# Performance work log

Measured on AMD Instinct MI355X. Metric: run time of the kernel, lower is better.

The kernel has to match this reference:

```python
import jax, jax.numpy as jnp
import numpy as np

QUERY_DIM = 1024
HIDDEN_DIM = 1024


def setup_inputs() -> dict:
    key = jax.random.key(0)
    k1, k2, k3, k4 = jax.random.split(key, 4)
    query = jax.random.normal(k1, (8, 2048, QUERY_DIM), dtype=jnp.float32)
    info = jax.random.normal(k2, (8, 2048, HIDDEN_DIM), dtype=jnp.float32)
    # nn.Linear params: weight [out, in], bias [out]
    bound = 1.0 / np.sqrt(QUERY_DIM)
    W = jax.random.uniform(k3, (HIDDEN_DIM, QUERY_DIM), jnp.float32, -bound, bound)
    b = jax.random.uniform(k4, (HIDDEN_DIM,), jnp.float32, -bound, bound)
    return {"query": query, "info": info, "W": W, "b": b}


def reference(query, info, W, b):
    # Eval mode: dropout is identity.
    # projected query: [B, S, hidden]
    q = jnp.einsum("bsq,hq->bsh", query, W) + b
    # unscaled attention scores over info rows: [B, S, M]
    scores = jax.nn.softmax(jnp.einsum("bsh,bmh->bsm", q, info), axis=-1)
    # weighted sum of info: [B, S, hidden]
    return jnp.einsum("bsm,bmh->bsh", scores, info)
```

## Files before the change

### kernel.cpp

```cpp
#include <hip/hip_runtime.h>

#define DEVI __device__ __forceinline__

typedef __attribute__((ext_vector_type(4))) float f32x4;
typedef __attribute__((ext_vector_type(8))) short bf16x8;

typedef const unsigned __attribute__((address_space(1))) as1_u32;
typedef unsigned __attribute__((address_space(3))) as3_u32;

DEVI unsigned fbits(float x){ union{float f;unsigned u;} v; v.f=x; return v.u; }
DEVI float bitsf(unsigned u){ union{unsigned u;float f;} v; v.u=u; return v.f; }
DEVI short bf_rne(float x){ unsigned u=fbits(x); u += 0x7fffu + ((u>>16)&1u); return (short)(u>>16); }

DEVI unsigned pack_hi2(unsigned u0, unsigned u1){
#if __has_builtin(__builtin_amdgcn_perm)
  return __builtin_amdgcn_perm(u1, u0, 0x07060302u);
#else
  return (u0 >> 16) | (u1 & 0xffff0000u);
#endif
}
DEVI unsigned pack_rne2(float a, float b){
  return (unsigned)(unsigned short)bf_rne(a) | ((unsigned)(unsigned short)bf_rne(b) << 16);
}

DEVI void gload16(const short* g, short* s){
  __builtin_amdgcn_global_load_lds((as1_u32*)g, (as3_u32*)s, 16, 0, 0);
}

#define SBAR() { __builtin_amdgcn_sched_barrier(0); asm volatile("" ::: "memory"); \
                 __builtin_amdgcn_s_barrier(); __builtin_amdgcn_sched_barrier(0); }

#define MF(a,b,c) __builtin_amdgcn_mfma_f32_16x16x32_bf16(a,b,c,0,0,0)
#define MROW(M, x) \
  acc[M][0] = MF(x, bb0, acc[M][0]); \
  acc[M][1] = MF(x, bb1, acc[M][1]); \
  acc[M][2] = MF(x, bb2, acc[M][2]); \
  acc[M][3] = MF(x, bb3, acc[M][3]);

__global__ __launch_bounds__(256)
void k_split(const float* __restrict__ in, short* __restrict__ hi,
             short* __restrict__ lo, const long n4)
{
  long i = (long)blockIdx.x*256 + threadIdx.x;
  const long stride = (long)gridDim.x*256;
  for (; i < n4; i += stride){
    const float4 v = ((const float4*)in)[i];
    const unsigned u0=fbits(v.x), u1=fbits(v.y), u2=fbits(v.z), u3=fbits(v.w);
    ((uint2*)hi)[i] = make_uint2(pack_hi2(u0,u1), pack_hi2(u2,u3));
    const float l0 = v.x - bitsf(u0 & 0xffff0000u);
    const float l1 = v.y - bitsf(u1 & 0xffff0000u);
    const float l2 = v.z - bitsf(u2 & 0xffff0000u);
    const float l3 = v.w - bitsf(u3 & 0xffff0000u);
    ((uint2*)lo)[i] = make_uint2(pack_rne2(l0,l1), pack_rne2(l2,l3));
  }
}

template<int NPHASE, bool BIAS, bool SPLIT_OUT>
__global__ __launch_bounds__(512, 2)
void k_gemm(const short* __restrict__ Ah, const short* __restrict__ Al,
            const short* __restrict__ Bh, const short* __restrict__ Bl,
            void* __restrict__ Cv, const float* __restrict__ bias,
            const int K, const int lda, const int ldb, const int ldc,
            const long sAz, const long sBz, const long sCz, const int loOff)
{
  __shared__ short LDS[65536];

  const int tid = threadIdx.x;
  const int w = tid >> 6, l = tid & 63;
  const int wr = w >> 2, wc = w & 3;
  const int fr = l & 15, h4 = l >> 4;
  const long bz = blockIdx.z;

  const int nwg = gridDim.x * gridDim.y;
  const int xy  = blockIdx.y * gridDim.x + blockIdx.x;
  const int q8  = nwg >> 3;
  const int sw  = (xy & 7) * q8 + (xy >> 3);
  const int bx  = sw % gridDim.x;
  const int by  = sw / gridDim.x;

  const size_t aOff = (size_t)bz*sAz + (size_t)bx*256*lda;
  const size_t bOff = (size_t)bz*sBz + (size_t)by*256*ldb;

  const int sch = (((l & 7) ^ ((l >> 3) & 7)) << 3);
  const int rA0 = wr*128 + (w & 3)*8 + (l >> 3);
  int aoffg[4];
#pragma unroll
  for (int q2 = 0; q2 < 4; ++q2) aoffg[q2] = (rA0 + 32*q2)*lda;
  const int rB0 = wc*64 + (w >> 2)*8 + (l >> 3);
  int boffg[4];
#pragma unroll
  for (int j2 = 0; j2 < 4; ++j2) boffg[j2] = (rB0 + 16*j2)*ldb;
  const int dAu = wr*8192 + (w & 3)*512;
  const int dBu = 16384 + wc*4096 + (w >> 2)*512;

  const int rbA = (wr*128 + fr)*64;
  const int rbB = 16384 + (wc*64 + fr)*64;
  const int c08 = ((h4     ) ^ (l & 7)) << 3;
  const int c18 = ((h4 + 4 ) ^ (l & 7)) << 3;

  f32x4 acc[8][4];
#pragma unroll
  for (int m = 0; m < 8; ++m)
#pragma unroll
    for (int n = 0; n < 4; ++n){ acc[m][n][0]=0.f; acc[m][n][1]=0.f; acc[m][n][2]=0.f; acc[m][n][3]=0.f; }

  const short* Asrc = Ah + aOff + sch;
  const short* Bsrc = Bh + bOff + sch;
  int skt = 0, spass = 0;
  const int nkt = NPHASE * (K >> 6);

  {
    short* dB0 = LDS + dBu;
    short* dA0 = LDS + dAu;
    gload16(Bsrc + boffg[0], dB0);
    gload16(Bsrc + boffg[1], dB0 + 1024);
    gload16(Bsrc + boffg[2], dB0 + 2048);
    gload16(Bsrc + boffg[3], dB0 + 3072);
    gload16(Asrc + aoffg[0], dA0);
    gload16(Asrc + aoffg[1], dA0 + 2048);
    gload16(Asrc + aoffg[2], dA0 + 4096);
    gload16(Asrc + aoffg[3], dA0 + 6144);
  }
  skt = 64; Asrc += 64; Bsrc += 64;
  asm volatile("s_waitcnt vmcnt(2)" ::: "memory");
  SBAR();

#define ADVANCE()                                                            \
  { skt += 64;                                                               \
    if (skt == K){ skt = 0; ++spass;                                         \
      Asrc = ((NPHASE==3 && spass==1) ? Al : Ah) + aOff + sch;               \
      Bsrc = ((NPHASE==3 && spass==2) ? Bl : Bh) + bOff + sch;               \
    } else { Asrc += 64; Bsrc += 64; } }

#define TILE(CO, PF, VA, VB)                                                 \
{                                                                            \
  const short* pA = LDS + (CO) + rbA;                                        \
  const short* pB = LDS + (CO) + rbB;                                        \
  short* dAp = LDS + ((CO)^32768) + dAu;                                     \
  short* dBp = LDS + ((CO)^32768) + dBu;                                     \
  bf16x8 aA,aB,aC,aD, bb0,bb1,bb2,bb3;                                       \
                                            \
  if (PF){ gload16(Bsrc + boffg[0], dBp); gload16(Bsrc + boffg[1], dBp + 1024); } \
  bb0 = *(const bf16x8*)(pB +        c08);                                   \
  bb1 = *(const bf16x8*)(pB + 1024 + c08);                                   \
  bb2 = *(const bf16x8*)(pB + 2048 + c08);                                   \
  bb3 = *(const bf16x8*)(pB + 3072 + c08);                                   \
  aA  = *(const bf16x8*)(pA +        c08);                                   \
  aB  = *(const bf16x8*)(pA + 1024 + c08);                                   \
  aC  = *(const bf16x8*)(pA + 2048 + c08);                                   \
  aD  = *(const bf16x8*)(pA + 3072 + c08);                                   \
  SBAR();                                                                    \
  __builtin_amdgcn_s_setprio(1);                                             \
  MROW(0,aA) MROW(1,aB) MROW(2,aC) MROW(3,aD)                                \
  __builtin_amdgcn_s_setprio(0);                                             \
  asm volatile("s_waitcnt vmcnt(" VA ")" ::: "memory");                      \
  SBAR();                                                                    \
                                                    \
  if (PF){ gload16(Bsrc + boffg[2], dBp + 2048); gload16(Bsrc + boffg[3], dBp + 3072); } \
  aA = *(const bf16x8*)(pA + 4096 + c08);                                    \
  aB = *(const bf16x8*)(pA + 5120 + c08);                                    \
  aC = *(const bf16x8*)(pA + 6144 + c08);                                    \
  aD = *(const bf16x8*)(pA + 7168 + c08);                                    \
  SBAR();                                                                    \
  __builtin_amdgcn_s_setprio(1);                                             \
  MROW(4,aA) MROW(5,aB) MROW(6,aC) MROW(7,aD)                                \
  __builtin_amdgcn_s_setprio(0);                                             \
  SBAR();                                                                    \
                                            \
  if (PF){ gload16(Asrc + aoffg[0], dAp); gload16(Asrc + aoffg[1], dAp + 2048); } \
  bb0 = *(const bf16x8*)(pB +        c18);                                   \
  bb1 = *(const bf16x8*)(pB + 1024 + c18);                                   \
  bb2 = *(const bf16x8*)(pB + 2048 + c18);                                   \
  bb3 = *(const bf16x8*)(pB + 3072 + c18);                                   \
  aA  = *(const bf16x8*)(pA +        c18);                                   \
  aB  = *(const bf16x8*)(pA + 1024 + c18);                                   \
  aC  = *(const bf16x8*)(pA + 2048 + c18);                                   \
  aD  = *(const bf16x8*)(pA + 3072 + c18);                                   \
  SBAR();                                                                    \
  __builtin_amdgcn_s_setprio(1);                                             \
  MROW(0,aA) MROW(1,aB) MROW(2,aC) MROW(3,aD)                                \
  __builtin_amdgcn_s_setprio(0);                                             \
  SBAR();                                                                    \
                                                    \
  if (PF){ gload16(Asrc + aoffg[2], dAp + 4096); gload16(Asrc + aoffg[3], dAp + 6144); } \
  aA = *(const bf16x8*)(pA + 4096 + c18);                                    \
  aB = *(const bf16x8*)(pA + 5120 + c18);                                    \
  aC = *(const bf16x8*)(pA + 6144 + c18);                                    \
  aD = *(const bf16x8*)(pA + 7168 + c18);                                    \
  SBAR();                                                                    \
  __builtin_amdgcn_s_setprio(1);                                             \
  MROW(4,aA) MROW(5,aB) MROW(6,aC) MROW(7,aD)                                \
  __builtin_amdgcn_s_setprio(0);                                             \
  if (PF){ ADVANCE(); }                                                      \
  asm volatile("s_waitcnt vmcnt(" VB ")" ::: "memory");                      \
  SBAR();                                                                    \
}

#pragma unroll 1
  for (int it = 0; it < nkt - 2; it += 2){
    TILE(0,     1, "2", "2")
    TILE(32768, 1, "2", "2")
  }
  TILE(0,     1, "2", "2")
  TILE(32768, 0, "0", "0")

#undef TILE
#undef ADVANCE

  const int rr = h4*4;
  if constexpr (SPLIT_OUT){
    short* Ch = (short*)Cv + (size_t)bz*sCz
              + (size_t)(bx*256 + wr*128)*ldc + by*256 + wc*64;
    short* Cl = Ch + loOff;
#pragma unroll
    for (int n = 0; n < 4; ++n){
      const int col = n*16 + fr;
      const float bv = BIAS ? bias[by*256 + wc*64 + col] : 0.f;
#pragma unroll
      for (int m = 0; m < 8; ++m)
#pragma unroll
        for (int j = 0; j < 4; ++j){
          const float v = acc[m][n][j] + bv;
          const unsigned uh = fbits(v) & 0xffff0000u;
          const size_t idx = (size_t)(m*16 + rr + j)*ldc + col;
          Ch[idx] = (short)(uh >> 16);
          Cl[idx] = bf_rne(v - bitsf(uh));
        }
    }
  } else {
    float* C = (float*)Cv + (size_t)bz*sCz
             + (size_t)(bx*256 + wr*128)*ldc + by*256 + wc*64;
#pragma unroll
    for (int n = 0; n < 4; ++n){
      const int col = n*16 + fr;
      const float bv = BIAS ? bias[by*256 + wc*64 + col] : 0.f;
#pragma unroll
      for (int m = 0; m < 8; ++m)
#pragma unroll
        for (int j = 0; j < 4; ++j)
          C[(size_t)(m*16 + rr + j)*ldc + col] = acc[m][n][j] + bv;
    }
  }
}

__global__ __launch_bounds__(256)
void k_prep_info(const float* __restrict__ V, short* __restrict__ hi,
                 short* __restrict__ lo, short* __restrict__ T,
                 const int MM, const int DD, const long sVz, const long sTz)
{
  __shared__ float t[64][65];
  const float* Vb = V + (long)blockIdx.z*sVz;
  short* hb = hi + (long)blockIdx.z*sVz;
  short* lb = lo + (long)blockIdx.z*sVz;
  short* Tb = T  + (long)blockIdx.z*sTz;
  const int m0 = blockIdx.x*64, d0 = blockIdx.y*64;
  const int tid = threadIdx.x;
#pragma unroll
  for (int i = 0; i < 4; ++i){
    const int c = tid + 256*i;
    const int r = c >> 4, c4 = (c & 15)*4;
    const float4 v = *(const float4*)(Vb + (size_t)(m0 + r)*DD + d0 + c4);
    t[r][c4+0]=v.x; t[r][c4+1]=v.y; t[r][c4+2]=v.z; t[r][c4+3]=v.w;
    const unsigned u0=fbits(v.x), u1=fbits(v.y), u2=fbits(v.z), u3=fbits(v.w);
    const size_t gi = (size_t)(m0 + r)*DD + d0 + c4;
    *(uint2*)(hb + gi) = make_uint2(pack_hi2(u0,u1), pack_hi2(u2,u3));
    const float l0 = v.x - bitsf(u0 & 0xffff0000u);
    const float l1 = v.y - bitsf(u1 & 0xffff0000u);
    const float l2 = v.z - bitsf(u2 & 0xffff0000u);
    const float l3 = v.w - bitsf(u3 & 0xffff0000u);
    *(uint2*)(lb + gi) = make_uint2(pack_rne2(l0,l1), pack_rne2(l2,l3));
  }
  __syncthreads();
#pragma unroll
  for (int i = 0; i < 4; ++i){
    const int c = tid + 256*i;
    const int d = c >> 4, m4 = (c & 15)*4;
    short4 o;
    o.x = bf_rne(t[m4+0][d]); o.y = bf_rne(t[m4+1][d]);
    o.z = bf_rne(t[m4+2][d]); o.w = bf_rne(t[m4+3][d]);
    *(short4*)(Tb + (size_t)(d0 + d)*MM + m0 + m4) = o;
  }
}

__global__ __launch_bounds__(256)
void k_softmax_rows(float* __restrict__ Sb, const long sz)
{
  float* row = Sb + (long)blockIdx.y*sz + (long)blockIdx.x*2048;
  short* prow = (short*)row;
  const int tid = threadIdx.x;
  const int lane = tid & 63, wid = tid >> 6;

  const float4 v0 = *(const float4*)(row + tid*4);
  const float4 v1 = *(const float4*)(row + 1024 + tid*4);
  float x[8] = {v0.x, v0.y, v0.z, v0.w, v1.x, v1.y, v1.z, v1.w};

  float mx = x[0];
#pragma unroll
  for (int j = 1; j < 8; ++j) mx = fmaxf(mx, x[j]);
#pragma unroll
  for (int off = 32; off; off >>= 1) mx = fmaxf(mx, __shfl_xor(mx, off));

  __shared__ float red[8];
  if (lane == 0) red[wid] = mx;
  __syncthreads();
  mx = fmaxf(fmaxf(red[0], red[1]), fmaxf(red[2], red[3]));

  float e[8]; float s = 0.f;
#pragma unroll
  for (int j = 0; j < 8; ++j){ e[j] = __expf(x[j] - mx); s += e[j]; }
#pragma unroll
  for (int off = 32; off; off >>= 1) s += __shfl_xor(s, off);
  if (lane == 0) red[4 + wid] = s;
  __syncthreads();
  s = (red[4] + red[5]) + (red[6] + red[7]);
  const float inv = 1.0f / s;

  *(uint2*)(prow + tid*4)        = make_uint2(pack_rne2(e[0]*inv, e[1]*inv), pack_rne2(e[2]*inv, e[3]*inv));
  *(uint2*)(prow + 1024 + tid*4) = make_uint2(pack_rne2(e[4]*inv, e[5]*inv), pack_rne2(e[6]*inv, e[7]*inv));
}

extern "C" void kernel_launch(void* const* d_in, const int* in_sizes, int n_in,
                              void* d_out, int out_size, void* d_ws, size_t ws_size,
                              hipStream_t stream)
{
  const float* query = (const float*)d_in[0];
  const float* info  = (const float*)d_in[1];
  const float* Wm    = (const float*)d_in[2];
  const float* bias  = (const float*)d_in[3];
  float* out = (float*)d_out;

  const int B = 8, S = 2048, M = 2048, D = 1024;
  const size_t PB = (size_t)S * D;

  short* info_hi = (short*)d_ws;
  short* info_lo = info_hi + 16777216;
  short* infoT   = info_lo + 16777216;
  short* W_hi    = infoT   + 16777216;
  short* W_lo    = W_hi    + 1048576;
  float* Sbuf    = (float*)(W_lo + 1048576);
  const size_t sb = (size_t)S * M * sizeof(float);
  size_t avail = ws_size > 104857600ull ? ws_size - 104857600ull : 0;
  int nchunk = (int)(avail / sb); if (nchunk > 8) nchunk = 8; if (nchunk < 1) nchunk = 1;

  short* q_s = (short*)d_out;
  const long qBz = 2*(long)PB;
  const int  qLo = (int)PB;

  k_split<<<1024, 256, 0, stream>>>(Wm, W_hi, W_lo, (long)(D*D/4));

  int nb = 2*nchunk; if (nb > 8) nb = 8;
  for (int q0 = 0; q0 < B; q0 += nb){
    const int cur = (q0 + nb <= B) ? nb : (B - q0);
    short* qt_hi = (short*)Sbuf;
    short* qt_lo = qt_hi + (size_t)cur*PB;
    k_split<<<2048, 256, 0, stream>>>(query + (size_t)q0*PB, qt_hi, qt_lo,
                                      (long)((size_t)cur*PB/4));
    k_gemm<3, true, true><<<dim3(S/256, D/256, cur), 512, 0, stream>>>(
        qt_hi, qt_lo, W_hi, W_lo, q_s + (size_t)q0*qBz, bias,
        D, D, D, D, (long)PB, 0L, qBz, qLo);
  }

  k_prep_info<<<dim3(M/64, D/64, B), 256, 0, stream>>>(
      info, info_hi, info_lo, infoT, M, D, (long)PB, (long)PB);

  for (int b0 = 0; b0 < B; b0 += nchunk){
    const int cur = (b0 + nchunk <= B) ? nchunk : (B - b0);

    const short* qh = q_s + (size_t)b0*qBz;
    k_gemm<3, false, false><<<dim3(S/256, M/256, cur), 512, 0, stream>>>(
        qh, qh + qLo, info_hi + (size_t)b0*PB, info_lo + (size_t)b0*PB,
        Sbuf, nullptr, D, D, D, M, qBz, (long)PB, (long)S*M, 0);

    k_softmax_rows<<<dim3(S, cur), 256, 0, stream>>>(Sbuf, (long)S*M);

    k_gemm<1, false, false><<<dim3(S/256, D/256, cur), 512, 0, stream>>>(
        (const short*)Sbuf, nullptr, infoT + (size_t)b0*PB, nullptr,
        out + (size_t)b0*PB, nullptr, M, 2*M, M, D,
        (long)(2*(size_t)S*M), (long)PB, (long)PB, 0);
  }
}
```

Baseline: 450.6 us.

## Fuse three bf16 split passes into single K loop reusing LDS fragments

```diff
diff --git a/kernel.cpp b/kernel.cpp
--- a/kernel.cpp
+++ b/kernel.cpp
@@ -55,13 +55,13 @@
   }
 }
 
-template<int NPHASE, bool BIAS, bool SPLIT_OUT>
+template<bool BIAS, bool SPLIT_OUT>
 __global__ __launch_bounds__(512, 2)
-void k_gemm(const short* __restrict__ Ah, const short* __restrict__ Al,
-            const short* __restrict__ Bh, const short* __restrict__ Bl,
-            void* __restrict__ Cv, const float* __restrict__ bias,
-            const int K, const int lda, const int ldb, const int ldc,
-            const long sAz, const long sBz, const long sCz, const int loOff)
+void k_gemm3(const short* __restrict__ Ah, const short* __restrict__ Al,
+             const short* __restrict__ Bh, const short* __restrict__ Bl,
+             void* __restrict__ Cv, const float* __restrict__ bias,
+             const int K, const int lda, const int ldb, const int ldc,
+             const long sAz, const long sBz, const long sCz, const int loOff)
 {
   __shared__ short LDS[65536];
 
@@ -81,6 +81,172 @@
   const size_t aOff = (size_t)bz*sAz + (size_t)bx*256*lda;
   const size_t bOff = (size_t)bz*sBz + (size_t)by*256*ldb;
 
+  const int c0 = w*64 + l, c1 = c0 + 512;
+  const size_t a0 = (size_t)(c0 >> 2)*lda + (c0 & 3)*8;
+  const size_t a1 = (size_t)(c1 >> 2)*lda + (c1 & 3)*8;
+  const size_t b0 = (size_t)(c0 >> 2)*ldb + (c0 & 3)*8;
+  const size_t b1 = (size_t)(c1 >> 2)*ldb + (c1 & 3)*8;
+  const int dS0 = w*512, dS1 = 4096 + w*512;
+
+  const int rbA = (wr*128 + fr)*32 + h4*8;
+  const int rbB = 16384 + (wc*64 + fr)*32 + h4*8;
+
+  f32x4 acc[8][4];
+#pragma unroll
+  for (int m = 0; m < 8; ++m)
+#pragma unroll
+    for (int n = 0; n < 4; ++n){ acc[m][n][0]=0.f; acc[m][n][1]=0.f; acc[m][n][2]=0.f; acc[m][n][3]=0.f; }
+
+  const short* pAh = Ah + aOff;
+  const short* pAl = Al + aOff;
+  const short* pBh = Bh + bOff;
+  const short* pBl = Bl + bOff;
+
+  gload16(pAh + a0, LDS + dS0);
+  gload16(pAh + a1, LDS + dS1);
+  gload16(pBh + b0, LDS + 16384 + dS0);
+  gload16(pBh + b1, LDS + 16384 + dS1);
+  gload16(pAl + a0, LDS + 8192 + dS0);
+  gload16(pAl + a1, LDS + 8192 + dS1);
+  gload16(pBl + b0, LDS + 24576 + dS0);
+  gload16(pBl + b1, LDS + 24576 + dS1);
+  pAh += 32; pAl += 32; pBh += 32; pBl += 32;
+
+#define STEP3(CO, PF, V1, V2, V3)                                            \
+{                                                                            \
+  const short* pA = LDS + (CO) + rbA;                                        \
+  const short* pB = LDS + (CO) + rbB;                                        \
+  short* dst = LDS + ((CO) ^ 32768);                                         \
+  bf16x8 ah0,ah1,ah2,ah3,ah4,ah5,ah6,ah7, bb0,bb1,bb2,bb3;                   \
+                                                            \
+  asm volatile("s_waitcnt vmcnt(" V1 ")" ::: "memory");                      \
+  SBAR();                                                                    \
+  if (PF){ gload16(pAh + a0, dst + dS0);                                     \
+           gload16(pAh + a1, dst + dS1);                                     \
+           gload16(pBh + b0, dst + 16384 + dS0);                             \
+           gload16(pBh + b1, dst + 16384 + dS1); }                           \
+  bb0 = *(const bf16x8*)(pB);                                                \
+  bb1 = *(const bf16x8*)(pB + 512);                                          \
+  bb2 = *(const bf16x8*)(pB + 1024);                                         \
+  bb3 = *(const bf16x8*)(pB + 1536);                                         \
+  ah0 = *(const bf16x8*)(pA);                                                \
+  ah1 = *(const bf16x8*)(pA + 512);                                          \
+  ah2 = *(const bf16x8*)(pA + 1024);                                         \
+  ah3 = *(const bf16x8*)(pA + 1536);                                         \
+  ah4 = *(const bf16x8*)(pA + 2048);                                         \
+  ah5 = *(const bf16x8*)(pA + 2560);                                         \
+  ah6 = *(const bf16x8*)(pA + 3072);                                         \
+  ah7 = *(const bf16x8*)(pA + 3584);                                         \
+  __builtin_amdgcn_s_setprio(1);                                             \
+  MROW(0,ah0) MROW(1,ah1) MROW(2,ah2) MROW(3,ah3)                            \
+  MROW(4,ah4) MROW(5,ah5) MROW(6,ah6) MROW(7,ah7)                            \
+  __builtin_amdgcn_s_setprio(0);                                             \
+                                                            \
+  asm volatile("s_waitcnt vmcnt(" V2 ")" ::: "memory");                      \
+  SBAR();                                                                    \
+  if (PF){ gload16(pAl + a0, dst + 8192 + dS0);                              \
+           gload16(pAl + a1, dst + 8192 + dS1);                              \
+           gload16(pBl + b0, dst + 24576 + dS0);                             \
+           gload16(pBl + b1, dst + 24576 + dS1);                             \
+           pAh += 32; pAl += 32; pBh += 32; pBl += 32; }                     \
+  {                                                                          \
+    bf16x8 al0 = *(const bf16x8*)(pA + 8192);                                \
+    bf16x8 al1 = *(const bf16x8*)(pA + 8192 + 512);                          \
+    bf16x8 al2 = *(const bf16x8*)(pA + 8192 + 1024);                         \
+    bf16x8 al3 = *(const bf16x8*)(pA + 8192 + 1536);                         \
+    bf16x8 al4 = *(const bf16x8*)(pA + 8192 + 2048);                         \
+    bf16x8 al5 = *(const bf16x8*)(pA + 8192 + 2560);                         \
+    bf16x8 al6 = *(const bf16x8*)(pA + 8192 + 3072);                         \
+    bf16x8 al7 = *(const bf16x8*)(pA + 8192 + 3584);                         \
+    __builtin_amdgcn_s_setprio(1);                                           \
+    MROW(0,al0) MROW(1,al1) MROW(2,al2) MROW(3,al3)                          \
+    MROW(4,al4) MROW(5,al5) MROW(6,al6) MROW(7,al7)                          \
+    __builtin_amdgcn_s_setprio(0);                                           \
+  }                                                                          \
+                                                            \
+  asm volatile("s_waitcnt vmcnt(" V3 ")" ::: "memory");                      \
+  SBAR();                                                                    \
+  bb0 = *(const bf16x8*)(pB + 8192);                                         \
+  bb1 = *(const bf16x8*)(pB + 8192 + 512);                                   \
+  bb2 = *(const bf16x8*)(pB + 8192 + 1024);                                  \
+  bb3 = *(const bf16x8*)(pB + 8192 + 1536);                                  \
+  __builtin_amdgcn_s_setprio(1);                                             \
+  MROW(0,ah0) MROW(1,ah1) MROW(2,ah2) MROW(3,ah3)                            \
+  MROW(4,ah4) MROW(5,ah5) MROW(6,ah6) MROW(7,ah7)                            \
+  __builtin_amdgcn_s_setprio(0);                                             \
+}
+
+  const int nk = K >> 5;
+#pragma unroll 1
+  for (int it = 0; it < nk - 2; it += 2){
+    STEP3(0,     1, "4", "6", "8")
+    STEP3(32768, 1, "4", "6", "8")
+  }
+  STEP3(0,     1, "4", "6", "8")
+  STEP3(32768, 0, "4", "2", "0")
+
+#undef STEP3
+
+  const int rr = h4*4;
+  if constexpr (SPLIT_OUT){
+    short* Ch = (short*)Cv + (size_t)bz*sCz
+              + (size_t)(bx*256 + wr*128)*ldc + by*256 + wc*64;
+    short* Cl = Ch + loOff;
+#pragma unroll
+    for (int n = 0; n < 4; ++n){
+      const int col = n*16 + fr;
+      const float bv = BIAS ? bias[by*256 + wc*64 + col] : 0.f;
+#pragma unroll
+      for (int m = 0; m < 8; ++m)
+#pragma unroll
+        for (int j = 0; j < 4; ++j){
+          const float v = acc[m][n][j] + bv;
+          const unsigned uh = fbits(v) & 0xffff0000u;
+          const size_t idx = (size_t)(m*16 + rr + j)*ldc + col;
+          Ch[idx] = (short)(uh >> 16);
+          Cl[idx] = bf_rne(v - bitsf(uh));
+        }
+    }
+  } else {
+    float* C = (float*)Cv + (size_t)bz*sCz
+             + (size_t)(bx*256 + wr*128)*ldc + by*256 + wc*64;
+#pragma unroll
+    for (int n = 0; n < 4; ++n){
+      const int col = n*16 + fr;
+      const float bv = BIAS ? bias[by*256 + wc*64 + col] : 0.f;
+#pragma unroll
+      for (int m = 0; m < 8; ++m)
+#pragma unroll
+        for (int j = 0; j < 4; ++j)
+          C[(size_t)(m*16 + rr + j)*ldc + col] = acc[m][n][j] + bv;
+    }
+  }
+}
+
+__global__ __launch_bounds__(512, 2)
+void k_gemm1(const short* __restrict__ Ah, const short* __restrict__ Bh,
+             void* __restrict__ Cv,
+             const int K, const int lda, const int ldb, const int ldc,
+             const long sAz, const long sBz, const long sCz)
+{
+  __shared__ short LDS[65536];
+
+  const int tid = threadIdx.x;
+  const int w = tid >> 6, l = tid & 63;
+  const int wr = w >> 2, wc = w & 3;
+  const int fr = l & 15, h4 = l >> 4;
+  const long bz = blockIdx.z;
+
+  const int nwg = gridDim.x * gridDim.y;
+  const int xy  = blockIdx.y * gridDim.x + blockIdx.x;
+  const int q8  = nwg >> 3;
+  const int sw  = (xy & 7) * q8 + (xy >> 3);
+  const int bx  = sw % gridDim.x;
+  const int by  = sw / gridDim.x;
+
+  const size_t aOff = (size_t)bz*sAz + (size_t)bx*256*lda;
+  const size_t bOff = (size_t)bz*sBz + (size_t)by*256*ldb;
+
   const int sch = (((l & 7) ^ ((l >> 3) & 7)) << 3);
   const int rA0 = wr*128 + (w & 3)*8 + (l >> 3);
   int aoffg[4];
@@ -106,8 +272,6 @@
 
   const short* Asrc = Ah + aOff + sch;
   const short* Bsrc = Bh + bOff + sch;
-  int skt = 0, spass = 0;
-  const int nkt = NPHASE * (K >> 6);
 
   {
     short* dB0 = LDS + dBu;
@@ -121,16 +285,9 @@
     gload16(Asrc + aoffg[2], dA0 + 4096);
     gload16(Asrc + aoffg[3], dA0 + 6144);
   }
-  skt = 64; Asrc += 64; Bsrc += 64;
+  Asrc += 64; Bsrc += 64;
   asm volatile("s_waitcnt vmcnt(2)" ::: "memory");
   SBAR();
-
-#define ADVANCE()                                                            \
-  { skt += 64;                                                               \
-    if (skt == K){ skt = 0; ++spass;                                         \
-      Asrc = ((NPHASE==3 && spass==1) ? Al : Ah) + aOff + sch;               \
-      Bsrc = ((NPHASE==3 && spass==2) ? Bl : Bh) + bOff + sch;               \
-    } else { Asrc += 64; Bsrc += 64; } }
 
 #define TILE(CO, PF, VA, VB)                                                 \
 {                                                                            \
@@ -139,7 +296,6 @@
   short* dAp = LDS + ((CO)^32768) + dAu;                                     \
   short* dBp = LDS + ((CO)^32768) + dBu;                                     \
   bf16x8 aA,aB,aC,aD, bb0,bb1,bb2,bb3;                                       \
-                                            \
   if (PF){ gload16(Bsrc + boffg[0], dBp); gload16(Bsrc + boffg[1], dBp + 1024); } \
   bb0 = *(const bf16x8*)(pB +        c08);                                   \
   bb1 = *(const bf16x8*)(pB + 1024 + c08);                                   \
@@ -155,7 +311,6 @@
   __builtin_amdgcn_s_setprio(0);                                             \
   asm volatile("s_waitcnt vmcnt(" VA ")" ::: "memory");                      \
   SBAR();                                                                    \
-                                                    \
   if (PF){ gload16(Bsrc + boffg[2], dBp + 2048); gload16(Bsrc + boffg[3], dBp + 3072); } \
   aA = *(const bf16x8*)(pA + 4096 + c08);                                    \
   aB = *(const bf16x8*)(pA + 5120 + c08);                                    \
@@ -166,7 +321,6 @@
   MROW(4,aA) MROW(5,aB) MROW(6,aC) MROW(7,aD)                                \
   __builtin_amdgcn_s_setprio(0);                                             \
   SBAR();                                                                    \
-                                            \
   if (PF){ gload16(Asrc + aoffg[0], dAp); gload16(Asrc + aoffg[1], dAp + 2048); } \
   bb0 = *(const bf16x8*)(pB +        c18);                                   \
   bb1 = *(const bf16x8*)(pB + 1024 + c18);                                   \
@@ -181,7 +335,6 @@
   MROW(0,aA) MROW(1,aB) MROW(2,aC) MROW(3,aD)                                \
   __builtin_amdgcn_s_setprio(0);                                             \
   SBAR();                                                                    \
-                                                    \
   if (PF){ gload16(Asrc + aoffg[2], dAp + 4096); gload16(Asrc + aoffg[3], dAp + 6144); } \
   aA = *(const bf16x8*)(pA + 4096 + c18);                                    \
   aB = *(const bf16x8*)(pA + 5120 + c18);                                    \
@@ -191,11 +344,12 @@
   __builtin_amdgcn_s_setprio(1);                                             \
   MROW(4,aA) MROW(5,aB) MROW(6,aC) MROW(7,aD)                                \
   __builtin_amdgcn_s_setprio(0);                                             \
-  if (PF){ ADVANCE(); }                                                      \
+  if (PF){ Asrc += 64; Bsrc += 64; }                                         \
   asm volatile("s_waitcnt vmcnt(" VB ")" ::: "memory");                      \
   SBAR();                                                                    \
 }
 
+  const int nkt = K >> 6;
 #pragma unroll 1
   for (int it = 0; it < nkt - 2; it += 2){
     TILE(0,     1, "2", "2")
@@ -205,41 +359,18 @@
   TILE(32768, 0, "0", "0")
 
 #undef TILE
-#undef ADVANCE
 
   const int rr = h4*4;
-  if constexpr (SPLIT_OUT){
-    short* Ch = (short*)Cv + (size_t)bz*sCz
-              + (size_t)(bx*256 + wr*128)*ldc + by*256 + wc*64;
-    short* Cl = Ch + loOff;
-#pragma unroll
-    for (int n = 0; n < 4; ++n){
-      const int col = n*16 + fr;
-      const float bv = BIAS ? bias[by*256 + wc*64 + col] : 0.f;
-#pragma unroll
-      for (int m = 0; m < 8; ++m)
-#pragma unroll
-        for (int j = 0; j < 4; ++j){
-          const float v = acc[m][n][j] + bv;
-          const unsigned uh = fbits(v) & 0xffff0000u;
-          const size_t idx = (size_t)(m*16 + rr + j)*ldc + col;
-          Ch[idx] = (short)(uh >> 16);
-          Cl[idx] = bf_rne(v - bitsf(uh));
-        }
-    }
-  } else {
-    float* C = (float*)Cv + (size_t)bz*sCz
-             + (size_t)(bx*256 + wr*128)*ldc + by*256 + wc*64;
-#pragma unroll
-    for (int n = 0; n < 4; ++n){
-      const int col = n*16 + fr;
-      const float bv = BIAS ? bias[by*256 + wc*64 + col] : 0.f;
-#pragma unroll
-      for (int m = 0; m < 8; ++m)
-#pragma unroll
-        for (int j = 0; j < 4; ++j)
-          C[(size_t)(m*16 + rr + j)*ldc + col] = acc[m][n][j] + bv;
-    }
+  float* C = (float*)Cv + (size_t)bz*sCz
+           + (size_t)(bx*256 + wr*128)*ldc + by*256 + wc*64;
+#pragma unroll
+  for (int n = 0; n < 4; ++n){
+    const int col = n*16 + fr;
+#pragma unroll
+    for (int m = 0; m < 8; ++m)
+#pragma unroll
+      for (int j = 0; j < 4; ++j)
+        C[(size_t)(m*16 + rr + j)*ldc + col] = acc[m][n][j];
   }
 }
 
@@ -355,7 +486,7 @@
     short* qt_lo = qt_hi + (size_t)cur*PB;
     k_split<<<2048, 256, 0, stream>>>(query + (size_t)q0*PB, qt_hi, qt_lo,
                                       (long)((size_t)cur*PB/4));
-    k_gemm<3, true, true><<<dim3(S/256, D/256, cur), 512, 0, stream>>>(
+    k_gemm3<true, true><<<dim3(S/256, D/256, cur), 512, 0, stream>>>(
         qt_hi, qt_lo, W_hi, W_lo, q_s + (size_t)q0*qBz, bias,
         D, D, D, D, (long)PB, 0L, qBz, qLo);
   }
@@ -367,15 +498,15 @@
     const int cur = (b0 + nchunk <= B) ? nchunk : (B - b0);
 
     const short* qh = q_s + (size_t)b0*qBz;
-    k_gemm<3, false, false><<<dim3(S/256, M/256, cur), 512, 0, stream>>>(
+    k_gemm3<false, false><<<dim3(S/256, M/256, cur), 512, 0, stream>>>(
         qh, qh + qLo, info_hi + (size_t)b0*PB, info_lo + (size_t)b0*PB,
         Sbuf, nullptr, D, D, D, M, qBz, (long)PB, (long)S*M, 0);
 
     k_softmax_rows<<<dim3(S, cur), 256, 0, stream>>>(Sbuf, (long)S*M);
 
-    k_gemm<1, false, false><<<dim3(S/256, D/256, cur), 512, 0, stream>>>(
-        (const short*)Sbuf, nullptr, infoT + (size_t)b0*PB, nullptr,
-        out + (size_t)b0*PB, nullptr, M, 2*M, M, D,
-        (long)(2*(size_t)S*M), (long)PB, (long)PB, 0);
-  }
-}
+    k_gemm1<<<dim3(S/256, D/256, cur), 512, 0, stream>>>(
+        (const short*)Sbuf, infoT + (size_t)b0*PB,
+        out + (size_t)b0*PB, M, 2*M, M, D,
+        (long)(2*(size_t)S*M), (long)PB, (long)S*D);
+  }
+}
```

New measurement: 449.4 us. No clear change (-0.3%).
